# Optimization experiments

Measured on AMD Instinct MI355X. Metric: run time of the kernel, lower is better.

## Reference

```python
import jax, jax.numpy as jnp
import numpy as np

HID = 16  # hidden channels of each lifting subnet (P and U)


def _conv(x, W, b):
    # x: [N,1|HID,h,w], W: [O,I,3,3] -> SAME conv, NCHW
    y = jax.lax.conv_general_dilated(x, W, (1, 1), 'SAME',
                                     dimension_numbers=('NCHW', 'OIHW', 'NCHW'))
    return y + b[None, :, None, None]


def _subnet(x, W1, b1, W2, b2):
    return _conv(jax.nn.relu(_conv(x, W1, b1)), W2, b2)


def _lift(L, H, p, u):
    # predict/update lifting step: H -= P(L); L += U(H)
    H = H - _subnet(L, *p)
    L = L + _subnet(H, *u)
    return L, H


def _rgb2yuv(x):
    # [B,3,H,W] -> YUV, then channels folded into batch -> [3B,1,H,W]
    M = jnp.array([[0.299, 0.587, 0.114],
                   [-0.147, -0.289, 0.436],
                   [0.615, -0.515, -0.100]], dtype=x.dtype)
    y = jnp.einsum('cd,bdhw->bchw', M, x)
    B, C, H, W = y.shape
    return y.transpose(1, 0, 2, 3).reshape(C * B, 1, H, W)


def _batch2channel(x, C):
    # [C*B,1,h,w] -> [B,C,h,w]  (inverse of the batch-fold above)
    CB, _, h, w = x.shape
    B = CB // C
    return x.reshape(C, B, h, w).transpose(1, 0, 2, 3)


def setup_inputs():
    key = jax.random.key(0)
    ks = jax.random.split(key, 5)
    B, H, W = 8, 512, 512
    x = jax.random.normal(ks[0], (B, 3, H, W), jnp.float32)

    def w(k, shape, fan):
        return jax.random.normal(k, shape, jnp.float32) * (1.0 / np.sqrt(fan))

    Wp1 = w(ks[1], (HID, 1, 3, 3), 9)
    bp1 = jnp.zeros((HID,), jnp.float32)
    Wp2 = w(ks[2], (1, HID, 3, 3), 9 * HID)
    bp2 = jnp.zeros((1,), jnp.float32)
    Wu1 = w(ks[3], (HID, 1, 3, 3), 9)
    bu1 = jnp.zeros((HID,), jnp.float32)
    Wu2 = w(ks[4], (1, HID, 3, 3), 9 * HID)
    bu2 = jnp.zeros((1,), jnp.float32)
    return dict(x=x, Wp1=Wp1, bp1=bp1, Wp2=Wp2, bp2=bp2,
                Wu1=Wu1, bu1=bu1, Wu2=Wu2, bu2=bu2)


def reference(x, Wp1, bp1, Wp2, bp2, Wu1, bu1, Wu2, bu2):
    p = (Wp1, bp1, Wp2, bp2)
    u = (Wu1, bu1, Wu2, bu2)
    C = x.shape[1]  # 3
    y = _rgb2yuv(x)                              # [3B,1,H,W]
    # level-1 vertical split + lifting
    L, Hb = y[:, :, 0::2, :], y[:, :, 1::2, :]   # [3B,1,H/2,W]
    L, Hb = _lift(L, Hb, p, u)
    # horizontal split of L
    Lt = L.transpose(0, 1, 3, 2)                 # [3B,1,W,H/2]
    LL, HL = Lt[:, :, 0::2, :], Lt[:, :, 1::2, :]
    LL, HL = _lift(LL, HL, p, u)
    LL = LL.transpose(0, 1, 3, 2)                # [3B,1,H/2,W/2]
    HL = HL.transpose(0, 1, 3, 2)
    # horizontal split of H
    Ht = Hb.transpose(0, 1, 3, 2)
    LH, HH = Ht[:, :, 0::2, :], Ht[:, :, 1::2, :]
    LH, HH = _lift(LH, HH, p, u)
    LH = LH.transpose(0, 1, 3, 2)
    HH = HH.transpose(0, 1, 3, 2)
    return jnp.concatenate([_batch2channel(t, C) for t in (LL, HL, LH, HH)],
                           axis=1)                # [B,12,H/2,W/2]
```

## Files before the change

kernel.cpp:

```cpp
#include <hip/hip_runtime.h>
#include <hip/hip_fp16.h>


#define P1 (24*256*512)

__device__ __forceinline__ __half2 oddpair(__half2 a, __half2 b) {
  unsigned ua = __builtin_bit_cast(unsigned, a), ub = __builtin_bit_cast(unsigned, b);
  unsigned r = __builtin_amdgcn_alignbit(ub, ua, 16);
  return __builtin_bit_cast(__half2, r);
}

__device__ __forceinline__ __half2 relu2(__half2 s) {
  unsigned u = __builtin_bit_cast(unsigned, s), r;
  asm("v_pk_max_f16 %0, %1, 0" : "=v"(r) : "v"(u));
  return __builtin_bit_cast(__half2, r);
}

__device__ __forceinline__ void load20(__half2 (&wv)[20], const __half2* src) {
  const float4* wq = (const float4*)src;
#pragma unroll
  for (int q = 0; q < 5; ++q) {
    float4 f = wq[q];
    wv[4*q+0] = __builtin_bit_cast(__half2, f.x);
    wv[4*q+1] = __builtin_bit_cast(__half2, f.y);
    wv[4*q+2] = __builtin_bit_cast(__half2, f.z);
    wv[4*q+3] = __builtin_bit_cast(__half2, f.w);
  }
}

__device__ __forceinline__ void channel_pass(
    const __half2 (&wv)[20],
    const __half2 (&E)[8][4], const __half2 (&O)[8][3],
    const bool (&rowok)[6], const bool edgex, const __half2 (&mE)[3],
    __half2 (&ACC2)[4][2], const __half2 negb)
{
  __half2 bias[6];
#pragma unroll
  for (int k = 0; k < 6; ++k) bias[k] = rowok[k] ? wv[9] : negb;

#pragma unroll
  for (int kk = 0; kk < 6; ++kk) {
    __half2 HE[3];
#pragma unroll
    for (int p = 0; p < 3; ++p) {
      __half2 hs = bias[kk];
#pragma unroll
      for (int dy = 0; dy < 3; ++dy) {
        hs = __hfma2(wv[dy*3+0], E[kk+dy][p],   hs);
        hs = __hfma2(wv[dy*3+1], O[kk+dy][p],   hs);
        hs = __hfma2(wv[dy*3+2], E[kk+dy][p+1], hs);
      }
      HE[p] = relu2(hs);
    }
    if (edgex) {
      HE[0] = __hmul2(HE[0], mE[0]);
      HE[1] = __hmul2(HE[1], mE[1]);
      HE[2] = __hmul2(HE[2], mE[2]);
    }
    __half2 HO0 = oddpair(HE[0], HE[1]);
    __half2 HO1 = oddpair(HE[1], HE[2]);
#pragma unroll
    for (int dy = 0; dy < 3; ++dy) {
      const int r = kk - dy;
      if (r >= 0 && r < 4) {
#pragma unroll
        for (int cp = 0; cp < 2; ++cp) {
          __half2 a = ACC2[r][cp];
          a = __hfma2(wv[10+dy*3+0], HE[cp],           a);
          a = __hfma2(wv[10+dy*3+1], (cp ? HO1 : HO0), a);
          a = __hfma2(wv[10+dy*3+2], HE[cp+1],         a);
          ACC2[r][cp] = a;
        }
      }
    }
  }
}

template<int MODE>
__global__ __launch_bounds__(256, 3) void k_subnet(
    const float* __restrict__ xp, float* __restrict__ ws, float* __restrict__ outp,
    const float* __restrict__ W1, const float* __restrict__ B1,
    const float* __restrict__ W2, const float* __restrict__ B2)
{
  constexpr int  IW    = (MODE <= 1) ? 512 : 256;
  constexpr int  HW    = 256 * IW;
  constexpr float sign = (MODE == 0 || MODE == 2) ? -1.f : 1.f;
  constexpr int  TRANS = (MODE >= 2) ? 1 : 0;

  __shared__ __align__(16) __half2 sW[16*20];
  __shared__ __align__(16) __half  sIn[68*72];

  const int z     = blockIdx.z;
  const int n     = (MODE >= 2) ? (z % 24) : z;
  const int which = (MODE >= 2) ? (z / 24) : 0;
  const int c_ = n >> 3, b_ = n & 7;
  const int x0 = blockIdx.x * 64, y0 = blockIdx.y * 64;
  const int tid = threadIdx.x;
  float* Lw = ws;
  float* Hw = ws + P1;

  for (int i = tid; i < 320; i += 256) {
    int cc = i / 20, j = i - cc*20;
    float v = 0.f;
    if (j < 9)       { int jt = TRANS ? ((j%3)*3 + j/3) : j; v = W1[cc*9 + jt]; }
    else if (j == 9) v = B1[cc];
    else if (j < 19) { int k = j - 10; int jt = TRANS ? ((k%3)*3 + k/3) : k; v = W2[cc*9 + jt]; }
    __half h = __float2half(v);
    sW[i] = __halves2half2(h, h);
  }

  float m0 = 0.f, m1 = 0.f, m2 = 0.f;
  if (MODE == 0) {
    m0 = (c_==0) ? 0.299f : ((c_==1) ? -0.147f :  0.615f);
    m1 = (c_==0) ? 0.587f : ((c_==1) ? -0.289f : -0.515f);
    m2 = (c_==0) ? 0.114f : ((c_==1) ?  0.436f : -0.100f);
  }
  {
    int ly = tid / 68, lx = tid - (tid / 68) * 68;
    for (int i = tid; i < 68*68; i += 256) {
      int gy = y0 + ly - 2, gx = x0 + lx - 2;
      float v = 0.f;
      if ((unsigned)gy < 256u && (unsigned)gx < (unsigned)IW) {
        if (MODE == 0) {
          const float* xb = xp + ((long)b_*3*512 + 2*gy)*512 + gx;
          v = m0*xb[0] + m1*xb[262144] + m2*xb[524288];
          Lw[(long)n*HW + gy*IW + gx] = v;
        } else if (MODE == 1) {
          v = Hw[(long)n*HW + gy*IW + gx];
        } else if (MODE == 2) {
          const float* s = (which ? Hw : Lw) + (long)n*(256*512);
          v = s[gy*512 + 2*gx];
        } else {
          const float* s = outp + (long)(b_*12 + (which?9:3) + c_)*65536;
          v = s[gy*256 + gx];
        }
      }
      sIn[ly*72 + lx] = __float2half(v);
      lx += 52; ly += 3;
      if (lx >= 68) { lx -= 68; ++ly; }
    }
  }
  __syncthreads();

  const int tx = tid & 15, ty = tid >> 4;
  const int oy = y0 + ty*4, ox = x0 + tx*4;

  __half2 E[8][4], O[8][3];
#pragma unroll
  for (int r = 0; r < 8; ++r) {
    const __half2* row = (const __half2*)&sIn[(ty*4 + r)*72 + tx*4];
    E[r][0] = row[0]; E[r][1] = row[1]; E[r][2] = row[2]; E[r][3] = row[3];
    O[r][0] = oddpair(E[r][0], E[r][1]);
    O[r][1] = oddpair(E[r][1], E[r][2]);
    O[r][2] = oddpair(E[r][2], E[r][3]);
  }

  const bool edgex = (x0 == 0) || (x0 + 64 == IW);
  bool rowok[6];
#pragma unroll
  for (int k = 0; k < 6; ++k) rowok[k] = ((unsigned)(oy - 1 + k) < 256u);
  __half2 mE[3];
#pragma unroll
  for (int p = 0; p < 3; ++p) mE[p] = __builtin_bit_cast(__half2, 0u);
  if (edgex) {
#pragma unroll
    for (int p = 0; p < 3; ++p) {
      float a = ((unsigned)(ox - 1 + 2*p) < (unsigned)IW) ? 1.f : 0.f;
      float b = ((unsigned)(ox     + 2*p) < (unsigned)IW) ? 1.f : 0.f;
      mE[p] = __halves2half2(__float2half(a), __float2half(b));
    }
  }

  const __half2 zero2 = __builtin_bit_cast(__half2, 0u);
  const __half2 negb  = __halves2half2(__float2half(-60000.f), __float2half(-60000.f));

  float   ACCF[4][4] = {{0,0,0,0},{0,0,0,0},{0,0,0,0},{0,0,0,0}};
  __half2 ACC2[4][2] = {{zero2,zero2},{zero2,zero2},{zero2,zero2},{zero2,zero2}};

  __half2 wvA[20], wvB[20];
  load20(wvA, &sW[0]);
#pragma unroll 1
  for (int c = 0; c < 16; c += 2) {
    load20(wvB, &sW[(c+1)*20]);
    channel_pass(wvA, E, O, rowok, edgex, mE, ACC2, negb);
    load20(wvA, &sW[(((c+2) & 15))*20]);
    channel_pass(wvB, E, O, rowok, edgex, mE, ACC2, negb);
    if ((c & 3) == 2) {
#pragma unroll
      for (int r = 0; r < 4; ++r)
#pragma unroll
        for (int cp = 0; cp < 2; ++cp) {
          ACCF[r][2*cp]   += __low2float(ACC2[r][cp]);
          ACCF[r][2*cp+1] += __high2float(ACC2[r][cp]);
          ACC2[r][cp] = zero2;
        }
    }
  }

  const float b2 = B2[0];
  float4 iov[4];
  if (MODE == 0) {
#pragma unroll
    for (int r = 0; r < 4; ++r) {
      const float* xb = xp + ((long)b_*3*512 + (2*(oy+r)+1))*512 + ox;
      float4 rr = *(const float4*)&xb[0];
      float4 gg = *(const float4*)&xb[262144];
      float4 bb = *(const float4*)&xb[524288];
      iov[r] = make_float4(m0*rr.x + m1*gg.x + m2*bb.x,
                           m0*rr.y + m1*gg.y + m2*bb.y,
                           m0*rr.z + m1*gg.z + m2*bb.z,
                           m0*rr.w + m1*gg.w + m2*bb.w);
    }
  } else if (MODE == 1) {
    const float* s = Lw + (long)n*HW;
#pragma unroll
    for (int r = 0; r < 4; ++r) iov[r] = *(const float4*)&s[(oy+r)*IW + ox];
  } else {
    const float* s = (which ? Hw : Lw) + (long)n*(256*512);
#pragma unroll
    for (int r = 0; r < 4; ++r) {
      float4 a = *(const float4*)&s[(oy+r)*512 + 2*ox];
      float4 b = *(const float4*)&s[(oy+r)*512 + 2*ox + 4];
      iov[r] = (MODE == 2) ? make_float4(a.y, a.w, b.y, b.w)
                           : make_float4(a.x, a.z, b.x, b.z);
    }
  }

  float* dst;
  if      (MODE == 0) dst = Hw + (long)n*HW;
  else if (MODE == 1) dst = Lw + (long)n*HW;
  else if (MODE == 2) dst = outp + (long)(b_*12 + (which?9:3) + c_)*65536;
  else                dst = outp + (long)(b_*12 + (which?6:0) + c_)*65536;

#pragma unroll
  for (int r = 0; r < 4; ++r) {
    float4 v;
    v.x = iov[r].x + sign * (ACCF[r][0] + b2);
    v.y = iov[r].y + sign * (ACCF[r][1] + b2);
    v.z = iov[r].z + sign * (ACCF[r][2] + b2);
    v.w = iov[r].w + sign * (ACCF[r][3] + b2);
    *(float4*)&dst[(oy + r)*IW + ox] = v;
  }
}

extern "C" void kernel_launch(void* const* d_in, const int* in_sizes, int n_in,
                              void* d_out, int out_size, void* d_ws, size_t ws_size,
                              hipStream_t stream) {
  const float* x   = (const float*)d_in[0];
  const float* Wp1 = (const float*)d_in[1];
  const float* bp1 = (const float*)d_in[2];
  const float* Wp2 = (const float*)d_in[3];
  const float* bp2 = (const float*)d_in[4];
  const float* Wu1 = (const float*)d_in[5];
  const float* bu1 = (const float*)d_in[6];
  const float* Wu2 = (const float*)d_in[7];
  const float* bu2 = (const float*)d_in[8];
  float* out = (float*)d_out;
  float* ws  = (float*)d_ws;

  k_subnet<0><<<dim3(8,4,24), 256, 0, stream>>>(x, ws, out, Wp1, bp1, Wp2, bp2);
  k_subnet<1><<<dim3(8,4,24), 256, 0, stream>>>(x, ws, out, Wu1, bu1, Wu2, bu2);
  k_subnet<2><<<dim3(4,4,48), 256, 0, stream>>>(x, ws, out, Wp1, bp1, Wp2, bp2);
  k_subnet<3><<<dim3(4,4,48), 256, 0, stream>>>(x, ws, out, Wu1, bu1, Wu2, bu2);
}
```

Before: 252.1 us.

## Fuse predict and update lifting steps into one kernel per level

Merges the predict (H -= P(L)) and update (L += U(H)) subnets of each lifting step into a single kernel, so four launches become two. Each block loads the even and odd rows with a wider halo into shared memory. It computes the predicted H over an enlarged 68x68 region (289 tiles, with 33 threads doing a second tile), then runs the update from shared memory. This removes the global round trip of the intermediate H and the re-read of L, and loads are now float4-vectorised. The cost is about 13% extra halo compute for the predict pass, uneven per-thread work, and the loss of the double-buffered weight loads.

Result: no change. 252.5 us (+0.2%).

```diff
diff --git a/kernel.cpp b/kernel.cpp
--- a/kernel.cpp
+++ b/kernel.cpp
@@ -76,116 +76,223 @@
   }
 }
 
-template<int MODE>
-__global__ __launch_bounds__(256, 3) void k_subnet(
+template<int FUSE>
+__global__ __launch_bounds__(256, 3) void k_pair(
     const float* __restrict__ xp, float* __restrict__ ws, float* __restrict__ outp,
-    const float* __restrict__ W1, const float* __restrict__ B1,
-    const float* __restrict__ W2, const float* __restrict__ B2)
+    const float* __restrict__ Wp1, const float* __restrict__ bp1,
+    const float* __restrict__ Wp2, const float* __restrict__ bp2,
+    const float* __restrict__ Wu1, const float* __restrict__ bu1,
+    const float* __restrict__ Wu2, const float* __restrict__ bu2)
 {
-  constexpr int  IW    = (MODE <= 1) ? 512 : 256;
-  constexpr int  HW    = 256 * IW;
-  constexpr float sign = (MODE == 0 || MODE == 2) ? -1.f : 1.f;
-  constexpr int  TRANS = (MODE >= 2) ? 1 : 0;
-
-  __shared__ __align__(16) __half2 sW[16*20];
-  __shared__ __align__(16) __half  sIn[68*72];
-
-  const int z     = blockIdx.z;
-  const int n     = (MODE >= 2) ? (z % 24) : z;
-  const int which = (MODE >= 2) ? (z / 24) : 0;
+  constexpr int IW = FUSE ? 256 : 512;
+  constexpr unsigned IWu = (unsigned)IW;
+
+  __shared__ __align__(16) __half2 sWp[16*20];
+  __shared__ __align__(16) __half2 sWu[16*20];
+  __shared__ __align__(16) __half  sEven[72*72];
+  __shared__ __align__(16) __half  sOdd [68*72];
+
+  const int z = blockIdx.z;
+  const int n     = FUSE ? (z % 24) : z;
+  const int which = FUSE ? (z / 24) : 0;
   const int c_ = n >> 3, b_ = n & 7;
   const int x0 = blockIdx.x * 64, y0 = blockIdx.y * 64;
   const int tid = threadIdx.x;
   float* Lw = ws;
   float* Hw = ws + P1;
 
-  for (int i = tid; i < 320; i += 256) {
-    int cc = i / 20, j = i - cc*20;
+  for (int i = tid; i < 640; i += 256) {
+    int st = (i >= 320) ? 1 : 0, j2 = i - 320*st;
+    int cc = j2 / 20, j = j2 - cc*20;
+    const float* W1 = st ? Wu1 : Wp1;
+    const float* B1 = st ? bu1 : bp1;
+    const float* W2 = st ? Wu2 : Wp2;
     float v = 0.f;
-    if (j < 9)       { int jt = TRANS ? ((j%3)*3 + j/3) : j; v = W1[cc*9 + jt]; }
+    if (j < 9)       { int jt = FUSE ? ((j%3)*3 + j/3) : j; v = W1[cc*9 + jt]; }
     else if (j == 9) v = B1[cc];
-    else if (j < 19) { int k = j - 10; int jt = TRANS ? ((k%3)*3 + k/3) : k; v = W2[cc*9 + jt]; }
+    else if (j < 19) { int k = j - 10; int jt = FUSE ? ((k%3)*3 + k/3) : k; v = W2[cc*9 + jt]; }
     __half h = __float2half(v);
-    sW[i] = __halves2half2(h, h);
+    (st ? sWu : sWp)[j2] = __halves2half2(h, h);
   }
 
   float m0 = 0.f, m1 = 0.f, m2 = 0.f;
-  if (MODE == 0) {
+  if (FUSE == 0) {
     m0 = (c_==0) ? 0.299f : ((c_==1) ? -0.147f :  0.615f);
     m1 = (c_==0) ? 0.587f : ((c_==1) ? -0.289f : -0.515f);
     m2 = (c_==0) ? 0.114f : ((c_==1) ?  0.436f : -0.100f);
   }
+  const float* srcq = FUSE ? ((which ? Hw : Lw) + (long)n*131072) : nullptr;
+
+  for (int i = tid; i < 72*18; i += 256) {
+    int ly = i / 18, g = i - ly*18;
+    int gy = y0 + ly - 4, gx = x0 + 4*g - 4;
+    float4 f = make_float4(0.f, 0.f, 0.f, 0.f);
+    if ((unsigned)gy < 256u && (unsigned)gx < IWu) {
+      if (FUSE == 0) {
+        const float* xb = xp + (long)b_*786432 + (2*gy)*512 + gx;
+        float4 rr = *(const float4*)&xb[0];
+        float4 gg = *(const float4*)&xb[262144];
+        float4 bb = *(const float4*)&xb[524288];
+        f.x = m0*rr.x + m1*gg.x + m2*bb.x;
+        f.y = m0*rr.y + m1*gg.y + m2*bb.y;
+        f.z = m0*rr.z + m1*gg.z + m2*bb.z;
+        f.w = m0*rr.w + m1*gg.w + m2*bb.w;
+      } else {
+        const float* s = srcq + gy*512 + 2*gx;
+        float4 a = *(const float4*)&s[0];
+        float4 b = *(const float4*)&s[4];
+        f = make_float4(a.x, a.z, b.x, b.z);
+      }
+    }
+    __half2* d = (__half2*)&sEven[ly*72 + 4*g];
+    d[0] = __halves2half2(__float2half(f.x), __float2half(f.y));
+    d[1] = __halves2half2(__float2half(f.z), __float2half(f.w));
+  }
+  for (int i = tid; i < 68*18; i += 256) {
+    int ly = i / 18, g = i - ly*18;
+    int gy = y0 + ly - 2, gx = x0 + 4*g - 4;
+    float4 f = make_float4(0.f, 0.f, 0.f, 0.f);
+    if ((unsigned)gy < 256u && (unsigned)gx < IWu) {
+      if (FUSE == 0) {
+        const float* xb = xp + (long)b_*786432 + (2*gy + 1)*512 + gx;
+        float4 rr = *(const float4*)&xb[0];
+        float4 gg = *(const float4*)&xb[262144];
+        float4 bb = *(const float4*)&xb[524288];
+        f.x = m0*rr.x + m1*gg.x + m2*bb.x;
+        f.y = m0*rr.y + m1*gg.y + m2*bb.y;
+        f.z = m0*rr.z + m1*gg.z + m2*bb.z;
+        f.w = m0*rr.w + m1*gg.w + m2*bb.w;
+      } else {
+        const float* s = srcq + gy*512 + 2*gx;
+        float4 a = *(const float4*)&s[0];
+        float4 b = *(const float4*)&s[4];
+        f = make_float4(a.y, a.w, b.y, b.w);
+      }
+    }
+    __half2* d = (__half2*)&sOdd[ly*72 + 4*g];
+    d[0] = __halves2half2(__float2half(f.x), __float2half(f.y));
+    d[1] = __halves2half2(__float2half(f.z), __float2half(f.w));
+  }
+  __syncthreads();
+
+  const __half2 zero2 = __builtin_bit_cast(__half2, 0u);
+  const __half2 negb  = __halves2half2(__float2half(-60000.f), __float2half(-60000.f));
+  const float b2p = bp2[0];
+
+  auto processA = [&](int T) {
+    const int tyA = T / 17, txA = T - tyA*17;
+    const int oyA = y0 - 2 + 4*tyA, oxA = x0 - 2 + 4*txA;
+    __half2 E[8][4], O[8][3];
+#pragma unroll
+    for (int r = 0; r < 8; ++r) {
+      const __half2* row = (const __half2*)&sEven[(4*tyA + r)*72 + 4*txA];
+      E[r][0] = row[0]; E[r][1] = row[1]; E[r][2] = row[2]; E[r][3] = row[3];
+      O[r][0] = oddpair(E[r][0], E[r][1]);
+      O[r][1] = oddpair(E[r][1], E[r][2]);
+      O[r][2] = oddpair(E[r][2], E[r][3]);
+    }
+    bool rowokA[6];
+#pragma unroll
+    for (int k = 0; k < 6; ++k) rowokA[k] = ((unsigned)(oyA - 1 + k) < 256u);
+    const bool edgexT = (oxA <= 0) || (oxA >= IW - 4);
+    __half2 mEA[3];
+#pragma unroll
+    for (int p = 0; p < 3; ++p) mEA[p] = zero2;
+    if (edgexT) {
+#pragma unroll
+      for (int p = 0; p < 3; ++p) {
+        float a = ((unsigned)(oxA - 1 + 2*p) < IWu) ? 1.f : 0.f;
+        float b = ((unsigned)(oxA     + 2*p) < IWu) ? 1.f : 0.f;
+        mEA[p] = __halves2half2(__float2half(a), __float2half(b));
+      }
+    }
+    float   ACCF[4][4] = {{0,0,0,0},{0,0,0,0},{0,0,0,0},{0,0,0,0}};
+    __half2 ACC2[4][2] = {{zero2,zero2},{zero2,zero2},{zero2,zero2},{zero2,zero2}};
+#pragma unroll 1
+    for (int c = 0; c < 16; ++c) {
+      __half2 wv[20];
+      load20(wv, &sWp[c*20]);
+      channel_pass(wv, E, O, rowokA, edgexT, mEA, ACC2, negb);
+      if ((c & 3) == 3) {
+#pragma unroll
+        for (int r = 0; r < 4; ++r)
+#pragma unroll
+          for (int cp = 0; cp < 2; ++cp) {
+            ACCF[r][2*cp]   += __low2float(ACC2[r][cp]);
+            ACCF[r][2*cp+1] += __high2float(ACC2[r][cp]);
+            ACC2[r][cp] = zero2;
+          }
+      }
+    }
+#pragma unroll
+    for (int r = 0; r < 4; ++r) {
+      const int gy = oyA + r;
+      const bool gyok = (unsigned)gy < 256u;
+      __half2* iop = (__half2*)&sOdd[(4*tyA + r)*72 + 4*txA + 2];
+      __half2 i01 = iop[0], i23 = iop[1];
+      float o0 = __low2float (i01) - (ACCF[r][0] + b2p);
+      float o1 = __high2float(i01) - (ACCF[r][1] + b2p);
+      float o2 = __low2float (i23) - (ACCF[r][2] + b2p);
+      float o3 = __high2float(i23) - (ACCF[r][3] + b2p);
+      __half h0 = (gyok && (unsigned)(oxA+0) < IWu) ? __float2half(o0) : __half(0);
+      __half h1 = (gyok && (unsigned)(oxA+1) < IWu) ? __float2half(o1) : __half(0);
+      __half h2_ = (gyok && (unsigned)(oxA+2) < IWu) ? __float2half(o2) : __half(0);
+      __half h3 = (gyok && (unsigned)(oxA+3) < IWu) ? __float2half(o3) : __half(0);
+      iop[0] = __halves2half2(h0, h1);
+      iop[1] = __halves2half2(h2_, h3);
+    }
+  };
+  processA(tid);
+  if (tid < 33) processA(256 + tid);
+  __syncthreads();
+
+  const int tx = tid & 15, ty = tid >> 4;
+  const int oy = y0 + 4*ty, ox = x0 + 4*tx;
   {
-    int ly = tid / 68, lx = tid - (tid / 68) * 68;
-    for (int i = tid; i < 68*68; i += 256) {
-      int gy = y0 + ly - 2, gx = x0 + lx - 2;
-      float v = 0.f;
-      if ((unsigned)gy < 256u && (unsigned)gx < (unsigned)IW) {
-        if (MODE == 0) {
-          const float* xb = xp + ((long)b_*3*512 + 2*gy)*512 + gx;
-          v = m0*xb[0] + m1*xb[262144] + m2*xb[524288];
-          Lw[(long)n*HW + gy*IW + gx] = v;
-        } else if (MODE == 1) {
-          v = Hw[(long)n*HW + gy*IW + gx];
-        } else if (MODE == 2) {
-          const float* s = (which ? Hw : Lw) + (long)n*(256*512);
-          v = s[gy*512 + 2*gx];
-        } else {
-          const float* s = outp + (long)(b_*12 + (which?9:3) + c_)*65536;
-          v = s[gy*256 + gx];
-        }
-      }
-      sIn[ly*72 + lx] = __float2half(v);
-      lx += 52; ly += 3;
-      if (lx >= 68) { lx -= 68; ++ly; }
-    }
-  }
-  __syncthreads();
-
-  const int tx = tid & 15, ty = tid >> 4;
-  const int oy = y0 + ty*4, ox = x0 + tx*4;
+    float* pAdst = FUSE ? (outp + (long)(b_*12 + (which?9:3) + c_)*65536)
+                        : (Hw + (long)n*131072);
+#pragma unroll
+    for (int r = 0; r < 4; ++r) {
+      const __half2* q = (const __half2*)&sOdd[(4*ty + 2 + r)*72 + 4*tx + 4];
+      __half2 a = q[0], b = q[1];
+      float4 v = make_float4(__low2float(a), __high2float(a),
+                             __low2float(b), __high2float(b));
+      *(float4*)&pAdst[(oy + r)*IW + ox] = v;
+    }
+  }
 
   __half2 E[8][4], O[8][3];
 #pragma unroll
   for (int r = 0; r < 8; ++r) {
-    const __half2* row = (const __half2*)&sIn[(ty*4 + r)*72 + tx*4];
+    const __half2* row = (const __half2*)&sOdd[(4*ty + r)*72 + 4*tx + 2];
     E[r][0] = row[0]; E[r][1] = row[1]; E[r][2] = row[2]; E[r][3] = row[3];
     O[r][0] = oddpair(E[r][0], E[r][1]);
     O[r][1] = oddpair(E[r][1], E[r][2]);
     O[r][2] = oddpair(E[r][2], E[r][3]);
   }
-
+  bool rowok[6];
+#pragma unroll
+  for (int k = 0; k < 6; ++k) rowok[k] = ((unsigned)(oy - 1 + k) < 256u);
   const bool edgex = (x0 == 0) || (x0 + 64 == IW);
-  bool rowok[6];
-#pragma unroll
-  for (int k = 0; k < 6; ++k) rowok[k] = ((unsigned)(oy - 1 + k) < 256u);
   __half2 mE[3];
 #pragma unroll
-  for (int p = 0; p < 3; ++p) mE[p] = __builtin_bit_cast(__half2, 0u);
+  for (int p = 0; p < 3; ++p) mE[p] = zero2;
   if (edgex) {
 #pragma unroll
     for (int p = 0; p < 3; ++p) {
-      float a = ((unsigned)(ox - 1 + 2*p) < (unsigned)IW) ? 1.f : 0.f;
-      float b = ((unsigned)(ox     + 2*p) < (unsigned)IW) ? 1.f : 0.f;
+      float a = ((unsigned)(ox - 1 + 2*p) < IWu) ? 1.f : 0.f;
+      float b = ((unsigned)(ox     + 2*p) < IWu) ? 1.f : 0.f;
       mE[p] = __halves2half2(__float2half(a), __float2half(b));
     }
   }
-
-  const __half2 zero2 = __builtin_bit_cast(__half2, 0u);
-  const __half2 negb  = __halves2half2(__float2half(-60000.f), __float2half(-60000.f));
-
   float   ACCF[4][4] = {{0,0,0,0},{0,0,0,0},{0,0,0,0},{0,0,0,0}};
   __half2 ACC2[4][2] = {{zero2,zero2},{zero2,zero2},{zero2,zero2},{zero2,zero2}};
-
-  __half2 wvA[20], wvB[20];
-  load20(wvA, &sW[0]);
 #pragma unroll 1
-  for (int c = 0; c < 16; c += 2) {
-    load20(wvB, &sW[(c+1)*20]);
-    channel_pass(wvA, E, O, rowok, edgex, mE, ACC2, negb);
-    load20(wvA, &sW[(((c+2) & 15))*20]);
-    channel_pass(wvB, E, O, rowok, edgex, mE, ACC2, negb);
-    if ((c & 3) == 2) {
+  for (int c = 0; c < 16; ++c) {
+    __half2 wv[20];
+    load20(wv, &sWu[c*20]);
+    channel_pass(wv, E, O, rowok, edgex, mE, ACC2, negb);
+    if ((c & 3) == 3) {
 #pragma unroll
       for (int r = 0; r < 4; ++r)
 #pragma unroll
@@ -196,49 +303,18 @@
         }
     }
   }
-
-  const float b2 = B2[0];
-  float4 iov[4];
-  if (MODE == 0) {
-#pragma unroll
-    for (int r = 0; r < 4; ++r) {
-      const float* xb = xp + ((long)b_*3*512 + (2*(oy+r)+1))*512 + ox;
-      float4 rr = *(const float4*)&xb[0];
-      float4 gg = *(const float4*)&xb[262144];
-      float4 bb = *(const float4*)&xb[524288];
-      iov[r] = make_float4(m0*rr.x + m1*gg.x + m2*bb.x,
-                           m0*rr.y + m1*gg.y + m2*bb.y,
-                           m0*rr.z + m1*gg.z + m2*bb.z,
-                           m0*rr.w + m1*gg.w + m2*bb.w);
-    }
-  } else if (MODE == 1) {
-    const float* s = Lw + (long)n*HW;
-#pragma unroll
-    for (int r = 0; r < 4; ++r) iov[r] = *(const float4*)&s[(oy+r)*IW + ox];
-  } else {
-    const float* s = (which ? Hw : Lw) + (long)n*(256*512);
-#pragma unroll
-    for (int r = 0; r < 4; ++r) {
-      float4 a = *(const float4*)&s[(oy+r)*512 + 2*ox];
-      float4 b = *(const float4*)&s[(oy+r)*512 + 2*ox + 4];
-      iov[r] = (MODE == 2) ? make_float4(a.y, a.w, b.y, b.w)
-                           : make_float4(a.x, a.z, b.x, b.z);
-    }
-  }
-
-  float* dst;
-  if      (MODE == 0) dst = Hw + (long)n*HW;
-  else if (MODE == 1) dst = Lw + (long)n*HW;
-  else if (MODE == 2) dst = outp + (long)(b_*12 + (which?9:3) + c_)*65536;
-  else                dst = outp + (long)(b_*12 + (which?6:0) + c_)*65536;
-
+  const float b2u = bu2[0];
+  float* dst = FUSE ? (outp + (long)(b_*12 + (which?6:0) + c_)*65536)
+                    : (Lw + (long)n*131072);
 #pragma unroll
   for (int r = 0; r < 4; ++r) {
+    const __half2* iop = (const __half2*)&sEven[(4*ty + 4 + r)*72 + 4*tx + 4];
+    __half2 a = iop[0], b = iop[1];
     float4 v;
-    v.x = iov[r].x + sign * (ACCF[r][0] + b2);
-    v.y = iov[r].y + sign * (ACCF[r][1] + b2);
-    v.z = iov[r].z + sign * (ACCF[r][2] + b2);
-    v.w = iov[r].w + sign * (ACCF[r][3] + b2);
+    v.x = __low2float (a) + (ACCF[r][0] + b2u);
+    v.y = __high2float(a) + (ACCF[r][1] + b2u);
+    v.z = __low2float (b) + (ACCF[r][2] + b2u);
+    v.w = __high2float(b) + (ACCF[r][3] + b2u);
     *(float4*)&dst[(oy + r)*IW + ox] = v;
   }
 }
@@ -258,8 +334,8 @@
   float* out = (float*)d_out;
   float* ws  = (float*)d_ws;
 
-  k_subnet<0><<<dim3(8,4,24), 256, 0, stream>>>(x, ws, out, Wp1, bp1, Wp2, bp2);
-  k_subnet<1><<<dim3(8,4,24), 256, 0, stream>>>(x, ws, out, Wu1, bu1, Wu2, bu2);
-  k_subnet<2><<<dim3(4,4,48), 256, 0, stream>>>(x, ws, out, Wp1, bp1, Wp2, bp2);
-  k_subnet<3><<<dim3(4,4,48), 256, 0, stream>>>(x, ws, out, Wu1, bu1, Wu2, bu2);
-}
+  k_pair<0><<<dim3(8,4,24), 256, 0, stream>>>(x, ws, out,
+      Wp1, bp1, Wp2, bp2, Wu1, bu1, Wu2, bu2);
+  k_pair<1><<<dim3(4,4,48), 256, 0, stream>>>(x, ws, out,
+      Wp1, bp1, Wp2, bp2, Wu1, bu1, Wu2, bu2);
+}
```
